# Optimization experiments

Measured on AMD Instinct MI355X. Metric: run time of the kernel, lower is better.

Reference implementation:

```python
import jax, jax.numpy as jnp
import numpy as np

DIM = 64
NUM_EXPERTS = 4
EPS = 1e-6
RESIDUAL_WEIGHT = 0.1
ATTN_SCALE = DIM ** (-0.5)


def setup_inputs() -> dict:
    key = jax.random.key(0)
    ks = jax.random.split(key, 24)
    N, d = 8192, DIM
    w = lambda k, shape: jax.random.normal(k, shape, dtype=jnp.float32) * 0.05
    return {
        "z_real": jax.random.normal(ks[0], (N, d), dtype=jnp.float32),
        "z_imag": jax.random.normal(ks[1], (N, d), dtype=jnp.float32),
        # ComplexMoE
        "gate_W": w(ks[2], (NUM_EXPERTS, 2 * d)),
        "gate_b": jnp.zeros((NUM_EXPERTS,), jnp.float32),
        "exp_Wr": w(ks[3], (NUM_EXPERTS, d, d)),
        "exp_Wi": w(ks[4], (NUM_EXPERTS, d, d)),
        # ComplexLayerNorm
        "ln_scale": jnp.ones((d,), jnp.float32),
        "ln_shift": jnp.zeros((d,), jnp.float32),
        # ModReLU
        "mod_bias": jnp.zeros((d,), jnp.float32),
        # ContextAwareAttention
        "q_Wr": w(ks[5], (d, d)), "q_Wi": w(ks[6], (d, d)),
        "k_Wr": w(ks[7], (d, d)), "k_Wi": w(ks[8], (d, d)),
        "v_Wr": w(ks[9], (d, d)), "v_Wi": w(ks[10], (d, d)),
        "ctx_W": w(ks[11], (2 * d, 2 * d)),
        "ctx_b": jnp.zeros((2 * d,), jnp.float32),
        # residual / halt / stack heads
        "res_W": w(ks[12], (2 * d, 2 * d)),
        "res_b": jnp.zeros((2 * d,), jnp.float32),
        "halt_W": w(ks[13], (1, 2 * d)),
        "halt_b": jnp.full((1,), 2.0, jnp.float32),
        "stack_W": w(ks[14], (3, 2 * d)),
        "stack_b": jnp.zeros((3,), jnp.float32),
    }


def _clinear(xr, xi, Wr, Wi):
    # complex linear: (xr + i xi) @ (Wr + i Wi)^T
    rr = xr @ Wr.T - xi @ Wi.T
    ri = xi @ Wr.T + xr @ Wi.T
    return rr, ri


def reference(z_real, z_imag, gate_W, gate_b, exp_Wr, exp_Wi,
              ln_scale, ln_shift, mod_bias,
              q_Wr, q_Wi, k_Wr, k_Wi, v_Wr, v_Wi, ctx_W, ctx_b,
              res_W, res_b, halt_W, halt_b, stack_W, stack_b):
    d = DIM
    zf = jnp.concatenate([z_real, z_imag], axis=-1)  # [N, 2d]

    # --- ComplexMoE ---
    gw = jax.nn.softmax(zf @ gate_W.T + gate_b, axis=-1)  # [N, E]
    er = jnp.einsum('nd,ekd->nek', z_real, exp_Wr) - jnp.einsum('nd,ekd->nek', z_imag, exp_Wi)
    ei = jnp.einsum('nd,ekd->nek', z_imag, exp_Wr) + jnp.einsum('nd,ekd->nek', z_real, exp_Wi)
    mr = jnp.einsum('ne,nek->nk', gw, er)
    mi = jnp.einsum('ne,nek->nk', gw, ei)

    # --- ComplexLayerNorm (mag stats with unbiased var, phase preserved) ---
    mag = jnp.sqrt(mr * mr + mi * mi) + EPS
    mean = jnp.mean(mag, axis=-1, keepdims=True)
    var = jnp.var(mag, axis=-1, keepdims=True, ddof=1)
    nm = (mag - mean) / jnp.sqrt(var + EPS) * ln_scale + ln_shift
    phase = jnp.arctan2(mi, mr)
    lr = nm * jnp.cos(phase)
    li = nm * jnp.sin(phase)

    # --- ModReLU ---
    nrm = jnp.sqrt(lr * lr + li * li) + EPS
    s = jax.nn.relu(nrm + mod_bias) / nrm
    ar, ai = lr * s, li * s

    # --- ContextAwareAttention (context = original z) ---
    qr, qi = _clinear(ar, ai, q_Wr, q_Wi)
    kr, ki = _clinear(ar, ai, k_Wr, k_Wi)
    vr, vi = _clinear(ar, ai, v_Wr, v_Wi)
    qf = jnp.concatenate([qr, qi], axis=-1)
    cw = jax.nn.sigmoid(zf @ ctx_W.T + ctx_b)
    qf = qf * cw
    kf = jnp.concatenate([kr, ki], axis=-1)
    attn = jax.nn.softmax((qf @ kf.T) * ATTN_SCALE, axis=-1)  # [N, N]
    or_ = attn @ vr
    oi_ = attn @ vi

    # --- residual projection ---
    res = zf @ res_W.T + res_b
    pr = or_ + RESIDUAL_WEIGHT * res[..., :d]
    pi = oi_ + RESIDUAL_WEIGHT * res[..., d:]

    # --- halt / stack heads on L2-normalized flat state ---
    zf2 = jnp.concatenate([pr, pi], axis=-1)
    zn = zf2 / (jnp.linalg.norm(zf2, axis=-1, keepdims=True) + 1e-6)
    halt_logit = zn @ halt_W.T + halt_b
    stack_logits = zn @ stack_W.T + stack_b
    return pr, pi, halt_logit, stack_logits
```

## Files before the change

kernel.cpp:

```cpp
#include <hip/hip_runtime.h>
#include <math.h>

#define EPS_F 1e-6f
#define NCH   8
#define CHUNK 1024
#define TILES 32
#define QSC   (0.125f * 1.44269504088896340736f)

#define GATE_O 0
#define EWR_O  512
#define EWI_O  16896
#define QWR_O  33280
#define QWI_O  37376
#define KWR_O  41472
#define KWI_O  45568
#define VWR_O  49664
#define VWI_O  53760
#define CTX_O  57856
#define RES_O  74240
#define WTOT   90624

typedef __attribute__((ext_vector_type(8))) short short8;
typedef __attribute__((ext_vector_type(4))) float f32x4;
typedef unsigned short ushort_t;
typedef unsigned int uint_t;

__device__ __forceinline__ ushort_t f2bf(float x){
  uint_t u = __float_as_uint(x);
  u += 0x7fffu + ((u >> 16) & 1u);
  return (ushort_t)(u >> 16);
}
__device__ __forceinline__ float bf2f(ushort_t u){
  return __uint_as_float(((uint_t)u) << 16);
}
__device__ __forceinline__ uint_t pack2bf(float lo, float hi){
  return (uint_t)f2bf(lo) | ((uint_t)f2bf(hi) << 16);
}

__device__ __forceinline__ float wave_sum64(float v){
  #pragma unroll
  for (int m = 32; m > 0; m >>= 1) v += __shfl_xor(v, m, 64);
  return v;
}
__device__ __forceinline__ float qsum16(float v){
  #pragma unroll
  for (int m = 1; m < 16; m <<= 1) v += __shfl_xor(v, m, 64);
  return v;
}

__device__ __forceinline__ short8 neg8(short8 v){
  uint4 u = *reinterpret_cast<uint4*>(&v);
  u.x ^= 0x80008000u; u.y ^= 0x80008000u; u.z ^= 0x80008000u; u.w ^= 0x80008000u;
  return *reinterpret_cast<short8*>(&u);
}
__device__ __forceinline__ short8 ld8(const ushort_t* __restrict__ p){
  return *reinterpret_cast<const short8*>(p);
}

#define MFMA(a,b,c) __builtin_amdgcn_mfma_f32_16x16x32_bf16((a),(b),(c),0,0,0)

__global__ __launch_bounds__(256) void wconv_kernel(
    const float* __restrict__ gate_W, const float* __restrict__ exp_Wr,
    const float* __restrict__ exp_Wi,
    const float* __restrict__ q_Wr, const float* __restrict__ q_Wi,
    const float* __restrict__ k_Wr, const float* __restrict__ k_Wi,
    const float* __restrict__ v_Wr, const float* __restrict__ v_Wi,
    const float* __restrict__ ctx_W, const float* __restrict__ res_W,
    ushort_t* __restrict__ whi, ushort_t* __restrict__ wlo)
{
  int i = blockIdx.x * 256 + threadIdx.x;
  if (i >= WTOT) return;
  float v;
  if      (i < EWR_O) v = gate_W[i - GATE_O];
  else if (i < EWI_O) v = exp_Wr[i - EWR_O];
  else if (i < QWR_O) v = exp_Wi[i - EWI_O];
  else if (i < QWI_O) v = q_Wr[i - QWR_O];
  else if (i < KWR_O) v = q_Wi[i - QWI_O];
  else if (i < KWI_O) v = k_Wr[i - KWR_O];
  else if (i < VWR_O) v = k_Wi[i - KWI_O];
  else if (i < VWI_O) v = v_Wr[i - VWR_O];
  else if (i < CTX_O) v = v_Wi[i - VWI_O];
  else if (i < RES_O) v = ctx_W[i - CTX_O];
  else                v = res_W[i - RES_O];
  ushort_t h = f2bf(v);
  whi[i] = h;
  wlo[i] = f2bf(v - bf2f(h));
}

__global__ __launch_bounds__(256, 4) void prep_kernel(
    const float* __restrict__ z_real, const float* __restrict__ z_imag,
    const ushort_t* __restrict__ whi, const ushort_t* __restrict__ wlo,
    const float* __restrict__ gate_b,
    const float* __restrict__ ln_scale, const float* __restrict__ ln_shift,
    const float* __restrict__ mod_bias,
    const float* __restrict__ ctx_b, const float* __restrict__ res_b,
    ushort_t* __restrict__ qf, ushort_t* __restrict__ kf, ushort_t* __restrict__ vt,
    float* __restrict__ resb)
{
  const int tid  = threadIdx.x;
  const int lane = tid & 63;
  const int w    = tid >> 6;
  const int g    = lane >> 4;
  const int c    = lane & 15;
  const int row0 = blockIdx.x * 16;
  const int col  = w * 16 + c;
  const f32x4 z4 = {0.f, 0.f, 0.f, 0.f};

  __shared__ ushort_t s_xh[16][136];
  __shared__ ushort_t s_xl[16][136];
  __shared__ ushort_t s_a [16][136];
  __shared__ ushort_t s_tv[128][20];
  __shared__ float    s_red[4][16][2];

  {
    int rowl = tid >> 4;
    int col0 = (tid & 15) * 8;
    const float* src = (col0 < 64) ? (z_real + (size_t)(row0 + rowl) * 64 + col0)
                                   : (z_imag + (size_t)(row0 + rowl) * 64 + (col0 - 64));
    float4 a = *reinterpret_cast<const float4*>(src);
    float4 b = *reinterpret_cast<const float4*>(src + 4);
    float f[8] = {a.x, a.y, a.z, a.w, b.x, b.y, b.z, b.w};
    uint_t hp[4], lp[4];
    #pragma unroll
    for (int e = 0; e < 4; ++e){
      ushort_t h0 = f2bf(f[2*e]), h1 = f2bf(f[2*e+1]);
      hp[e] = (uint_t)h0 | ((uint_t)h1 << 16);
      lp[e] = (uint_t)f2bf(f[2*e]   - bf2f(h0)) |
              ((uint_t)f2bf(f[2*e+1] - bf2f(h1)) << 16);
    }
    uint4 uh; uh.x = hp[0]; uh.y = hp[1]; uh.z = hp[2]; uh.w = hp[3];
    uint4 ul; ul.x = lp[0]; ul.y = lp[1]; ul.z = lp[2]; ul.w = lp[3];
    *reinterpret_cast<uint4*>(&s_xh[rowl][col0]) = uh;
    *reinterpret_cast<uint4*>(&s_xl[rowl][col0]) = ul;
  }
  __syncthreads();

  short8 xh[4], xl[4];
  #pragma unroll
  for (int ks = 0; ks < 4; ++ks){
    xh[ks] = ld8(&s_xh[c][ks * 32 + g * 8]);
    xl[ks] = ld8(&s_xl[c][ks * 32 + g * 8]);
  }

  float gwv[4];
  {
    f32x4 ga = z4;
    #pragma unroll
    for (int ks = 0; ks < 4; ++ks){
      int off = GATE_O + (c & 3) * 128 + ks * 32 + g * 8;
      short8 wh = ld8(whi + off), wl = ld8(wlo + off);
      ga = MFMA(xh[ks], wh, ga);
      ga = MFMA(xl[ks], wh, ga);
      ga = MFMA(xh[ks], wl, ga);
    }
    float gb = gate_b[c & 3];
    #pragma unroll
    for (int r = 0; r < 4; ++r){
      float le = ga[r] + gb;
      float mx = fmaxf(le, __shfl_xor(le, 1, 64));
      mx = fmaxf(mx, __shfl_xor(mx, 2, 64));
      float ev = __expf(le - mx);
      float sm = ev + __shfl_xor(ev, 1, 64);
      sm += __shfl_xor(sm, 2, 64);
      gwv[r] = ev / sm;
    }
  }

  f32x4 mrr = z4, mri = z4;
  #pragma unroll
  for (int e = 0; e < 4; ++e){
    float gwr[4];
    #pragma unroll
    for (int r = 0; r < 4; ++r) gwr[r] = __shfl(gwv[r], g * 16 + e, 64);
    f32x4 er = z4, ei = z4;
    #pragma unroll
    for (int ks = 0; ks < 2; ++ks){
      int boff = e * 4096 + col * 64 + ks * 32 + g * 8;
      short8 wrh = ld8(whi + EWR_O + boff);
      short8 wrl = ld8(wlo + EWR_O + boff);
      short8 wih = ld8(whi + EWI_O + boff);
      short8 wil = ld8(wlo + EWI_O + boff);
      short8 wihn = neg8(wih), wiln = neg8(wil);
      er = MFMA(xh[ks],   wrh, er);   ei = MFMA(xh[ks+2], wrh, ei);
      er = MFMA(xl[ks],   wrh, er);   ei = MFMA(xl[ks+2], wrh, ei);
      er = MFMA(xh[ks],   wrl, er);   ei = MFMA(xh[ks+2], wrl, ei);
      er = MFMA(xh[ks+2], wihn, er);  ei = MFMA(xh[ks],   wih, ei);
      er = MFMA(xl[ks+2], wihn, er);  ei = MFMA(xl[ks],   wih, ei);
      er = MFMA(xh[ks+2], wiln, er);  ei = MFMA(xh[ks],   wil, ei);
    }
    #pragma unroll
    for (int r = 0; r < 4; ++r){
      mrr[r] = fmaf(gwr[r], er[r], mrr[r]);
      mri[r] = fmaf(gwr[r], ei[r], mri[r]);
    }
  }

  {
    float hh[4], mg[4];
    #pragma unroll
    for (int r = 0; r < 4; ++r){
      hh[r] = sqrtf(mrr[r] * mrr[r] + mri[r] * mri[r]);
      mg[r] = hh[r] + EPS_F;
    }
    #pragma unroll
    for (int r = 0; r < 4; ++r){
      float sx  = qsum16(mg[r]);
      float sxx = qsum16(mg[r] * mg[r]);
      if (c == 0){ s_red[w][g * 4 + r][0] = sx; s_red[w][g * 4 + r][1] = sxx; }
    }
    __syncthreads();
    float lsc = ln_scale[col], lsh = ln_shift[col], mb = mod_bias[col];
    #pragma unroll
    for (int r = 0; r < 4; ++r){
      int rr = g * 4 + r;
      float SX  = s_red[0][rr][0] + s_red[1][rr][0] + s_red[2][rr][0] + s_red[3][rr][0];
      float SXX = s_red[0][rr][1] + s_red[1][rr][1] + s_red[2][rr][1] + s_red[3][rr][1];
      float mean = SX * (1.0f / 64.0f);
      float var  = (SXX - SX * mean) * (1.0f / 63.0f);
      float istd = rsqrtf(var + EPS_F);
      float nm = (mg[r] - mean) * istd * lsc + lsh;
      float lr, li;
      if (hh[r] > 0.f){ float ih = 1.0f / hh[r]; lr = nm * mrr[r] * ih; li = nm * mri[r] * ih; }
      else            { lr = nm; li = 0.f; }
      float nrm = sqrtf(lr * lr + li * li) + EPS_F;
      float sf  = fmaxf(nrm + mb, 0.f) / nrm;
      s_a[rr][col]      = f2bf(lr * sf);
      s_a[rr][64 + col] = f2bf(li * sf);
    }
  }
  __syncthreads();

  f32x4 cwa[2];
  #pragma unroll
  for (int ii = 0; ii < 2; ++ii){
    int ct8 = w + ii * 4;
    f32x4 a = z4;
    #pragma unroll
    for (int ks = 0; ks < 4; ++ks)
      a = MFMA(xh[ks], ld8(whi + CTX_O + (ct8 * 16 + c) * 128 + ks * 32 + g * 8), a);
    float cb = ctx_b[ct8 * 16 + c];
    #pragma unroll
    for (int r = 0; r < 4; ++r) cwa[ii][r] = 1.0f / (1.0f + __expf(-(a[r] + cb)));
  }

  #pragma unroll
  for (int ii = 0; ii < 2; ++ii){
    int ct8 = w + ii * 4;
    f32x4 a = z4;
    #pragma unroll
    for (int ks = 0; ks < 4; ++ks)
      a = MFMA(xh[ks], ld8(whi + RES_O + (ct8 * 16 + c) * 128 + ks * 32 + g * 8), a);
    float rb = res_b[ct8 * 16 + c];
    #pragma unroll
    for (int r = 0; r < 4; ++r)
      resb[(size_t)(row0 + 4 * g + r) * 128 + ct8 * 16 + c] = 0.1f * (a[r] + rb);
  }

  short8 ar_[2], ai_[2], ain_[2];
  #pragma unroll
  for (int ks = 0; ks < 2; ++ks){
    ar_[ks]  = ld8(&s_a[c][ks * 32 + g * 8]);
    ai_[ks]  = ld8(&s_a[c][64 + ks * 32 + g * 8]);
    ain_[ks] = neg8(ai_[ks]);
  }

  #pragma unroll
  for (int mat = 0; mat < 3; ++mat){
    int roff = (mat == 0) ? QWR_O : (mat == 1) ? KWR_O : VWR_O;
    int ioff = (mat == 0) ? QWI_O : (mat == 1) ? KWI_O : VWI_O;
    f32x4 orr = z4, oii = z4;
    #pragma unroll
    for (int ks = 0; ks < 2; ++ks){
      int boff = col * 64 + ks * 32 + g * 8;
      short8 wrh = ld8(whi + roff + boff);
      short8 wrl = ld8(wlo + roff + boff);
      short8 wih = ld8(whi + ioff + boff);
      short8 wil = ld8(wlo + ioff + boff);
      orr = MFMA(ar_[ks],  wrh, orr);  oii = MFMA(ai_[ks], wrh, oii);
      orr = MFMA(ar_[ks],  wrl, orr);  oii = MFMA(ai_[ks], wrl, oii);
      orr = MFMA(ain_[ks], wih, orr);  oii = MFMA(ar_[ks], wih, oii);
      orr = MFMA(ain_[ks], wil, orr);  oii = MFMA(ar_[ks], wil, oii);
    }
    if (mat == 0){
      #pragma unroll
      for (int r = 0; r < 4; ++r){
        size_t row = row0 + 4 * g + r;
        qf[row * 128 + col]      = f2bf(orr[r] * cwa[0][r] * QSC);
        qf[row * 128 + 64 + col] = f2bf(oii[r] * cwa[1][r] * QSC);
      }
    } else if (mat == 1){
      #pragma unroll
      for (int r = 0; r < 4; ++r){
        size_t row = row0 + 4 * g + r;
        kf[row * 128 + col]      = f2bf(orr[r]);
        kf[row * 128 + 64 + col] = f2bf(oii[r]);
      }
    } else {
      #pragma unroll
      for (int r = 0; r < 4; ++r){
        s_tv[col][4 * g + r]      = f2bf(orr[r]);
        s_tv[64 + col][4 * g + r] = f2bf(oii[r]);
      }
    }
  }
  __syncthreads();

  {
    int d = tid >> 1, half = tid & 1;
    uint2 t0 = *reinterpret_cast<const uint2*>(&s_tv[d][half * 8]);
    uint2 t1 = *reinterpret_cast<const uint2*>(&s_tv[d][half * 8 + 4]);
    uint4 o; o.x = t0.x; o.y = t0.y; o.z = t1.x; o.w = t1.y;
    *reinterpret_cast<uint4*>(vt + (size_t)d * 8192 + row0 + half * 8) = o;
  }
}

__global__ __launch_bounds__(256, 4) void attn_mfma(
    const ushort_t* __restrict__ qf, const ushort_t* __restrict__ kf, const ushort_t* __restrict__ vt,
    ushort_t* __restrict__ pacc, float* __restrict__ pm, float* __restrict__ pl)
{
  const int tid  = threadIdx.x;
  const int lane = tid & 63;
  const int w    = tid >> 6;
  const int g    = lane >> 4;
  const int hl   = lane & 15;
  const int qb   = blockIdx.x & 127;
  const int jc   = blockIdx.x >> 7;
  const int q0   = qb * 64;
  const int qr   = q0 + w * 16 + hl;

  __shared__ ushort_t s_k[32][136];
  __shared__ ushort_t s_vt[128][40];
  __shared__ uint_t   s_p32[4][16][20];

  const int kjj0 = tid >> 4;
  const int kkk  = (tid & 15) * 8;
  const int vd0  = tid >> 2;
  const int vjo  = (tid & 3) * 8;

  short8 qfrag[4];
  #pragma unroll
  for (int kt = 0; kt < 4; ++kt)
    qfrag[kt] = *reinterpret_cast<const short8*>(qf + (size_t)qr * 128 + kt * 32 + g * 8);

  f32x4 oacc[8];
  #pragma unroll
  for (int dt = 0; dt < 8; ++dt) oacc[dt] = (f32x4){0.f, 0.f, 0.f, 0.f};
  float mrun = -3.0e38f, lrun = 0.f;

  const int jstart = jc * CHUNK;

  for (int t = 0; t < TILES; ++t){
    const int jb = jstart + t * 32;
    __syncthreads();
    #pragma unroll
    for (int i = 0; i < 2; ++i){
      *reinterpret_cast<uint4*>(&s_k[kjj0 + i * 16][kkk]) =
          *reinterpret_cast<const uint4*>(kf + (size_t)(jb + kjj0 + i * 16) * 128 + kkk);
      *reinterpret_cast<uint4*>(&s_vt[vd0 + i * 64][vjo]) =
          *reinterpret_cast<const uint4*>(vt + (size_t)(vd0 + i * 64) * 8192 + jb + vjo);
    }
    __syncthreads();

    f32x4 sacc[2];
    #pragma unroll
    for (int jt = 0; jt < 2; ++jt){
      sacc[jt] = (f32x4){0.f, 0.f, 0.f, 0.f};
      #pragma unroll
      for (int kt = 0; kt < 4; ++kt){
        short8 kfr = *reinterpret_cast<const short8*>(&s_k[jt * 16 + hl][kt * 32 + g * 8]);
        sacc[jt] = __builtin_amdgcn_mfma_f32_16x16x32_bf16(kfr, qfrag[kt], sacc[jt], 0, 0, 0);
      }
    }

    float t0 = fmaxf(fmaxf(fmaxf(sacc[0][0], sacc[0][1]), fmaxf(sacc[0][2], sacc[0][3])),
                     fmaxf(fmaxf(sacc[1][0], sacc[1][1]), fmaxf(sacc[1][2], sacc[1][3])));
    t0 = fmaxf(t0, __shfl_xor(t0, 16, 64));
    t0 = fmaxf(t0, __shfl_xor(t0, 32, 64));
    if (__any(t0 > mrun)){
      float mnew = fmaxf(mrun, t0);
      float fac  = exp2f(mrun - mnew);
      lrun *= fac;
      #pragma unroll
      for (int dt = 0; dt < 8; ++dt){
        oacc[dt][0] *= fac; oacc[dt][1] *= fac; oacc[dt][2] *= fac; oacc[dt][3] *= fac;
      }
      mrun = mnew;
    }
    float pe[2][4];
    float ps = 0.f;
    #pragma unroll
    for (int jt = 0; jt < 2; ++jt)
      #pragma unroll
      for (int r = 0; r < 4; ++r){
        float p = exp2f(sacc[jt][r] - mrun);
        pe[jt][r] = p;
        ps += p;
      }
    ps += __shfl_xor(ps, 16, 64);
    ps += __shfl_xor(ps, 32, 64);
    lrun += ps;

    {
      uint2 w0; w0.x = pack2bf(pe[0][0], pe[0][1]); w0.y = pack2bf(pe[0][2], pe[0][3]);
      uint2 w1; w1.x = pack2bf(pe[1][0], pe[1][1]); w1.y = pack2bf(pe[1][2], pe[1][3]);
      *reinterpret_cast<uint2*>(&s_p32[w][hl][2 * g])     = w0;
      *reinterpret_cast<uint2*>(&s_p32[w][hl][8 + 2 * g]) = w1;
    }
    short8 pfrag = *reinterpret_cast<const short8*>(&s_p32[w][hl][4 * g]);

    #pragma unroll
    for (int dt = 0; dt < 8; ++dt){
      short8 vfr = *reinterpret_cast<const short8*>(&s_vt[dt * 16 + hl][g * 8]);
      oacc[dt] = __builtin_amdgcn_mfma_f32_16x16x32_bf16(vfr, pfrag, oacc[dt], 0, 0, 0);
    }
  }

  #pragma unroll
  for (int dt = 0; dt < 8; ++dt){
    uint2 o;
    o.x = pack2bf(oacc[dt][0], oacc[dt][1]);
    o.y = pack2bf(oacc[dt][2], oacc[dt][3]);
    *reinterpret_cast<uint2*>(pacc + ((size_t)jc * 8192 + qr) * 128 + dt * 16 + 4 * g) = o;
  }
  if (g == 0){
    pm[jc * 8192 + qr] = mrun;
    pl[jc * 8192 + qr] = lrun;
  }
}

__global__ __launch_bounds__(256, 1) void combine_kernel(
    const ushort_t* __restrict__ pacc, const float* __restrict__ pm, const float* __restrict__ pl,
    const float* __restrict__ resb,
    const float* __restrict__ halt_W, const float* __restrict__ halt_b,
    const float* __restrict__ stack_W, const float* __restrict__ stack_b,
    float* __restrict__ out)
{
  const int tid  = threadIdx.x;
  const int lane = tid & 63;
  const int w    = tid >> 6;
  const int q    = blockIdx.x * 4 + w;

  float mv[NCH], M = -3.0e38f;
  #pragma unroll
  for (int c = 0; c < NCH; ++c){ mv[c] = pm[c * 8192 + q]; M = fmaxf(M, mv[c]); }
  float f[NCH]; float L = 0.f;
  #pragma unroll
  for (int c = 0; c < NCH; ++c){ f[c] = exp2f(mv[c] - M); L += pl[c * 8192 + q] * f[c]; }
  float invL = 1.0f / L;

  float o0 = 0.f, o1 = 0.f;
  #pragma unroll
  for (int c = 0; c < NCH; ++c){
    const ushort_t* pa = pacc + ((size_t)c * 8192 + q) * 128;
    o0 += bf2f(pa[lane])      * f[c];
    o1 += bf2f(pa[64 + lane]) * f[c];
  }
  o0 = o0 * invL + resb[(size_t)q * 128 + lane];
  o1 = o1 * invL + resb[(size_t)q * 128 + 64 + lane];
  out[(size_t)q * 64 + lane] = o0;
  out[(size_t)8192 * 64 + (size_t)q * 64 + lane] = o1;

  float ssq  = wave_sum64(o0 * o0 + o1 * o1);
  float invn = 1.0f / (sqrtf(ssq) + 1e-6f);
  float zn0 = o0 * invn, zn1 = o1 * invn;
  float hp = wave_sum64(zn0 * halt_W[lane]        + zn1 * halt_W[64 + lane]);
  float s0 = wave_sum64(zn0 * stack_W[lane]       + zn1 * stack_W[64 + lane]);
  float s1 = wave_sum64(zn0 * stack_W[128 + lane] + zn1 * stack_W[192 + lane]);
  float s2 = wave_sum64(zn0 * stack_W[256 + lane] + zn1 * stack_W[320 + lane]);
  if (lane == 0){
    out[1048576 + q] = hp + halt_b[0];
    out[1056768 + (size_t)q * 3 + 0] = s0 + stack_b[0];
    out[1056768 + (size_t)q * 3 + 1] = s1 + stack_b[1];
    out[1056768 + (size_t)q * 3 + 2] = s2 + stack_b[2];
  }
}

extern "C" void kernel_launch(void* const* d_in, const int* in_sizes, int n_in,
                              void* d_out, int out_size, void* d_ws, size_t ws_size,
                              hipStream_t stream){
  const float* z_real  = (const float*)d_in[0];
  const float* z_imag  = (const float*)d_in[1];
  const float* gate_W  = (const float*)d_in[2];
  const float* gate_b  = (const float*)d_in[3];
  const float* exp_Wr  = (const float*)d_in[4];
  const float* exp_Wi  = (const float*)d_in[5];
  const float* ln_scale= (const float*)d_in[6];
  const float* ln_shift= (const float*)d_in[7];
  const float* mod_bias= (const float*)d_in[8];
  const float* q_Wr    = (const float*)d_in[9];
  const float* q_Wi    = (const float*)d_in[10];
  const float* k_Wr    = (const float*)d_in[11];
  const float* k_Wi    = (const float*)d_in[12];
  const float* v_Wr    = (const float*)d_in[13];
  const float* v_Wi    = (const float*)d_in[14];
  const float* ctx_W   = (const float*)d_in[15];
  const float* ctx_b   = (const float*)d_in[16];
  const float* res_W   = (const float*)d_in[17];
  const float* res_b   = (const float*)d_in[18];
  const float* halt_W  = (const float*)d_in[19];
  const float* halt_b  = (const float*)d_in[20];
  const float* stack_W = (const float*)d_in[21];
  const float* stack_b = (const float*)d_in[22];

  ushort_t* qbf = (ushort_t*)d_ws;
  ushort_t* kbf = qbf + (size_t)8192*128;
  ushort_t* vtb = kbf + (size_t)8192*128;
  float* resb = (float*)(vtb + (size_t)8192*128);
  ushort_t* pacc = (ushort_t*)(resb + (size_t)8192*128);
  float* pm   = (float*)(pacc + (size_t)NCH*8192*128);
  float* pl   = pm   + NCH*8192;
  ushort_t* whi = (ushort_t*)(pl + NCH*8192);
  ushort_t* wlo = whi + WTOT;

  wconv_kernel<<<(WTOT + 255) / 256, 256, 0, stream>>>(gate_W, exp_Wr, exp_Wi,
      q_Wr, q_Wi, k_Wr, k_Wi, v_Wr, v_Wi, ctx_W, res_W, whi, wlo);
  prep_kernel<<<512, 256, 0, stream>>>(z_real, z_imag, whi, wlo, gate_b,
      ln_scale, ln_shift, mod_bias, ctx_b, res_b, qbf, kbf, vtb, resb);
  attn_mfma<<<128*NCH, 256, 0, stream>>>(qbf, kbf, vtb, pacc, pm, pl);
  combine_kernel<<<2048, 256, 0, stream>>>(pacc, pm, pl, resb,
      halt_W, halt_b, stack_W, stack_b, (float*)d_out);
}
```

Baseline: 122.3 us.

## Register-prefetch K/V tiles, raise split-K chunks to 16, add MFMA priority hints

The attention kernel now loads the next K/V tile into registers while the current tile is computed, so global latency overlaps with the MFMA work. The key dimension is split into 16 chunks instead of 8 when the workspace is large enough, which doubles the grid to fill more CUs. Occupancy hint is raised from 4 to 6, and s_setprio wraps the MFMA sections. The trade-off is more partial-result traffic and combine work, plus extra register pressure from the prefetch registers.

```diff
diff --git a/kernel.cpp b/kernel.cpp
--- a/kernel.cpp
+++ b/kernel.cpp
@@ -2,9 +2,6 @@
 #include <math.h>
 
 #define EPS_F 1e-6f
-#define NCH   8
-#define CHUNK 1024
-#define TILES 32
 #define QSC   (0.125f * 1.44269504088896340736f)
 
 #define GATE_O 0
@@ -314,10 +311,14 @@
   }
 }
 
-__global__ __launch_bounds__(256, 4) void attn_mfma(
+template<int NCH_T>
+__global__ __launch_bounds__(256, 6) void attn_mfma(
     const ushort_t* __restrict__ qf, const ushort_t* __restrict__ kf, const ushort_t* __restrict__ vt,
     ushort_t* __restrict__ pacc, float* __restrict__ pm, float* __restrict__ pl)
 {
+  constexpr int CHUNK_T = 8192 / NCH_T;
+  constexpr int TILES_T = CHUNK_T / 32;
+
   const int tid  = threadIdx.x;
   const int lane = tid & 63;
   const int w    = tid >> 6;
@@ -336,6 +337,10 @@
   const int kkk  = (tid & 15) * 8;
   const int vd0  = tid >> 2;
   const int vjo  = (tid & 3) * 8;
+  const int jstart = jc * CHUNK_T;
+
+  const ushort_t* kp = kf + (size_t)(jstart + kjj0) * 128 + kkk;
+  const ushort_t* vp = vt + (size_t)vd0 * 8192 + jstart + vjo;
 
   short8 qfrag[4];
   #pragma unroll
@@ -347,21 +352,29 @@
   for (int dt = 0; dt < 8; ++dt) oacc[dt] = (f32x4){0.f, 0.f, 0.f, 0.f};
   float mrun = -3.0e38f, lrun = 0.f;
 
-  const int jstart = jc * CHUNK;
-
-  for (int t = 0; t < TILES; ++t){
-    const int jb = jstart + t * 32;
+  uint4 kreg0 = *reinterpret_cast<const uint4*>(kp);
+  uint4 kreg1 = *reinterpret_cast<const uint4*>(kp + 16 * 128);
+  uint4 vreg0 = *reinterpret_cast<const uint4*>(vp);
+  uint4 vreg1 = *reinterpret_cast<const uint4*>(vp + (size_t)64 * 8192);
+  kp += 32 * 128; vp += 32;
+
+  for (int t = 0; t < TILES_T; ++t){
     __syncthreads();
-    #pragma unroll
-    for (int i = 0; i < 2; ++i){
-      *reinterpret_cast<uint4*>(&s_k[kjj0 + i * 16][kkk]) =
-          *reinterpret_cast<const uint4*>(kf + (size_t)(jb + kjj0 + i * 16) * 128 + kkk);
-      *reinterpret_cast<uint4*>(&s_vt[vd0 + i * 64][vjo]) =
-          *reinterpret_cast<const uint4*>(vt + (size_t)(vd0 + i * 64) * 8192 + jb + vjo);
+    *reinterpret_cast<uint4*>(&s_k[kjj0][kkk])       = kreg0;
+    *reinterpret_cast<uint4*>(&s_k[kjj0 + 16][kkk])  = kreg1;
+    *reinterpret_cast<uint4*>(&s_vt[vd0][vjo])       = vreg0;
+    *reinterpret_cast<uint4*>(&s_vt[vd0 + 64][vjo])  = vreg1;
+    if (t + 1 < TILES_T){
+      kreg0 = *reinterpret_cast<const uint4*>(kp);
+      kreg1 = *reinterpret_cast<const uint4*>(kp + 16 * 128);
+      vreg0 = *reinterpret_cast<const uint4*>(vp);
+      vreg1 = *reinterpret_cast<const uint4*>(vp + (size_t)64 * 8192);
+      kp += 32 * 128; vp += 32;
     }
     __syncthreads();
 
     f32x4 sacc[2];
+    __builtin_amdgcn_s_setprio(1);
     #pragma unroll
     for (int jt = 0; jt < 2; ++jt){
       sacc[jt] = (f32x4){0.f, 0.f, 0.f, 0.f};
@@ -371,6 +384,7 @@
         sacc[jt] = __builtin_amdgcn_mfma_f32_16x16x32_bf16(kfr, qfrag[kt], sacc[jt], 0, 0, 0);
       }
     }
+    __builtin_amdgcn_s_setprio(0);
 
     float t0 = fmaxf(fmaxf(fmaxf(sacc[0][0], sacc[0][1]), fmaxf(sacc[0][2], sacc[0][3])),
                      fmaxf(fmaxf(sacc[1][0], sacc[1][1]), fmaxf(sacc[1][2], sacc[1][3])));
@@ -408,11 +422,13 @@
     }
     short8 pfrag = *reinterpret_cast<const short8*>(&s_p32[w][hl][4 * g]);
 
+    __builtin_amdgcn_s_setprio(1);
     #pragma unroll
     for (int dt = 0; dt < 8; ++dt){
       short8 vfr = *reinterpret_cast<const short8*>(&s_vt[dt * 16 + hl][g * 8]);
       oacc[dt] = __builtin_amdgcn_mfma_f32_16x16x32_bf16(vfr, pfrag, oacc[dt], 0, 0, 0);
     }
+    __builtin_amdgcn_s_setprio(0);
   }
 
   #pragma unroll
@@ -428,6 +444,7 @@
   }
 }
 
+template<int NCH_T>
 __global__ __launch_bounds__(256, 1) void combine_kernel(
     const ushort_t* __restrict__ pacc, const float* __restrict__ pm, const float* __restrict__ pl,
     const float* __restrict__ resb,
@@ -440,17 +457,17 @@
   const int w    = tid >> 6;
   const int q    = blockIdx.x * 4 + w;
 
-  float mv[NCH], M = -3.0e38f;
-  #pragma unroll
-  for (int c = 0; c < NCH; ++c){ mv[c] = pm[c * 8192 + q]; M = fmaxf(M, mv[c]); }
-  float f[NCH]; float L = 0.f;
-  #pragma unroll
-  for (int c = 0; c < NCH; ++c){ f[c] = exp2f(mv[c] - M); L += pl[c * 8192 + q] * f[c]; }
+  float mv[NCH_T], M = -3.0e38f;
+  #pragma unroll
+  for (int c = 0; c < NCH_T; ++c){ mv[c] = pm[c * 8192 + q]; M = fmaxf(M, mv[c]); }
+  float f[NCH_T]; float L = 0.f;
+  #pragma unroll
+  for (int c = 0; c < NCH_T; ++c){ f[c] = exp2f(mv[c] - M); L += pl[c * 8192 + q] * f[c]; }
   float invL = 1.0f / L;
 
   float o0 = 0.f, o1 = 0.f;
   #pragma unroll
-  for (int c = 0; c < NCH; ++c){
+  for (int c = 0; c < NCH_T; ++c){
     const ushort_t* pa = pacc + ((size_t)c * 8192 + q) * 128;
     o0 += bf2f(pa[lane])      * f[c];
     o1 += bf2f(pa[64 + lane]) * f[c];
@@ -502,21 +519,38 @@
   const float* stack_W = (const float*)d_in[21];
   const float* stack_b = (const float*)d_in[22];
 
+  const size_t base_elems = (size_t)3 * 8192 * 128;
+  auto need = [&](int nch)->size_t{
+    size_t b = base_elems * 2;
+    b += (size_t)8192 * 128 * 4;
+    b += (size_t)nch * 8192 * 128 * 2;
+    b += (size_t)2 * nch * 8192 * 4;
+    b += (size_t)2 * WTOT * 2;
+    return b;
+  };
+  const int nch = (ws_size >= need(16)) ? 16 : 8;
+
   ushort_t* qbf = (ushort_t*)d_ws;
   ushort_t* kbf = qbf + (size_t)8192*128;
   ushort_t* vtb = kbf + (size_t)8192*128;
   float* resb = (float*)(vtb + (size_t)8192*128);
   ushort_t* pacc = (ushort_t*)(resb + (size_t)8192*128);
-  float* pm   = (float*)(pacc + (size_t)NCH*8192*128);
-  float* pl   = pm   + NCH*8192;
-  ushort_t* whi = (ushort_t*)(pl + NCH*8192);
+  float* pm   = (float*)(pacc + (size_t)nch*8192*128);
+  float* pl   = pm   + (size_t)nch*8192;
+  ushort_t* whi = (ushort_t*)(pl + (size_t)nch*8192);
   ushort_t* wlo = whi + WTOT;
 
   wconv_kernel<<<(WTOT + 255) / 256, 256, 0, stream>>>(gate_W, exp_Wr, exp_Wi,
       q_Wr, q_Wi, k_Wr, k_Wi, v_Wr, v_Wi, ctx_W, res_W, whi, wlo);
   prep_kernel<<<512, 256, 0, stream>>>(z_real, z_imag, whi, wlo, gate_b,
       ln_scale, ln_shift, mod_bias, ctx_b, res_b, qbf, kbf, vtb, resb);
-  attn_mfma<<<128*NCH, 256, 0, stream>>>(qbf, kbf, vtb, pacc, pm, pl);
-  combine_kernel<<<2048, 256, 0, stream>>>(pacc, pm, pl, resb,
-      halt_W, halt_b, stack_W, stack_b, (float*)d_out);
-}
+  if (nch == 16){
+    attn_mfma<16><<<128*16, 256, 0, stream>>>(qbf, kbf, vtb, pacc, pm, pl);
+    combine_kernel<16><<<2048, 256, 0, stream>>>(pacc, pm, pl, resb,
+        halt_W, halt_b, stack_W, stack_b, (float*)d_out);
+  } else {
+    attn_mfma<8><<<128*8, 256, 0, stream>>>(qbf, kbf, vtb, pacc, pm, pl);
+    combine_kernel<8><<<2048, 256, 0, stream>>>(pacc, pm, pl, resb,
+        halt_W, halt_b, stack_W, stack_b, (float*)d_out);
+  }
+}
```

After: 204.6 us. +67.3%, slower.

## Load K/V MFMA fragments directly from global memory instead of LDS staging

Applied to the files above, without the earlier changes.

The attention kernel no longer stages each K and V^T tile through shared memory. Each wave now reads its MFMA fragments straight from global memory through a helper, which removes the two block-wide barriers per tile and the LDS write/read traffic. It also raises wave priority around the MFMA sections with s_setprio. The trade-off is that all four waves fetch the same K/V data separately, so they rely on cache hits, and load latency is no longer hidden by cooperative staging.

```diff
diff --git a/kernel.cpp b/kernel.cpp
--- a/kernel.cpp
+++ b/kernel.cpp
@@ -328,49 +328,36 @@
   const int q0   = qb * 64;
   const int qr   = q0 + w * 16 + hl;
 
-  __shared__ ushort_t s_k[32][136];
-  __shared__ ushort_t s_vt[128][40];
-  __shared__ uint_t   s_p32[4][16][20];
-
-  const int kjj0 = tid >> 4;
-  const int kkk  = (tid & 15) * 8;
-  const int vd0  = tid >> 2;
-  const int vjo  = (tid & 3) * 8;
+  __shared__ uint_t s_p32[4][16][20];
+
+  const ushort_t* kbase = kf + (size_t)(jc * CHUNK + hl) * 128 + g * 8;
+  const ushort_t* vbase = vt + (size_t)hl * 8192 + jc * CHUNK + g * 8;
 
   short8 qfrag[4];
   #pragma unroll
   for (int kt = 0; kt < 4; ++kt)
-    qfrag[kt] = *reinterpret_cast<const short8*>(qf + (size_t)qr * 128 + kt * 32 + g * 8);
+    qfrag[kt] = ld8(qf + (size_t)qr * 128 + kt * 32 + g * 8);
 
   f32x4 oacc[8];
   #pragma unroll
   for (int dt = 0; dt < 8; ++dt) oacc[dt] = (f32x4){0.f, 0.f, 0.f, 0.f};
   float mrun = -3.0e38f, lrun = 0.f;
 
-  const int jstart = jc * CHUNK;
-
   for (int t = 0; t < TILES; ++t){
-    const int jb = jstart + t * 32;
-    __syncthreads();
-    #pragma unroll
-    for (int i = 0; i < 2; ++i){
-      *reinterpret_cast<uint4*>(&s_k[kjj0 + i * 16][kkk]) =
-          *reinterpret_cast<const uint4*>(kf + (size_t)(jb + kjj0 + i * 16) * 128 + kkk);
-      *reinterpret_cast<uint4*>(&s_vt[vd0 + i * 64][vjo]) =
-          *reinterpret_cast<const uint4*>(vt + (size_t)(vd0 + i * 64) * 8192 + jb + vjo);
-    }
-    __syncthreads();
+    const int jb = t * 32;
 
     f32x4 sacc[2];
+    __builtin_amdgcn_s_setprio(1);
     #pragma unroll
     for (int jt = 0; jt < 2; ++jt){
       sacc[jt] = (f32x4){0.f, 0.f, 0.f, 0.f};
       #pragma unroll
       for (int kt = 0; kt < 4; ++kt){
-        short8 kfr = *reinterpret_cast<const short8*>(&s_k[jt * 16 + hl][kt * 32 + g * 8]);
+        short8 kfr = ld8(kbase + (size_t)(jb + jt * 16) * 128 + kt * 32);
         sacc[jt] = __builtin_amdgcn_mfma_f32_16x16x32_bf16(kfr, qfrag[kt], sacc[jt], 0, 0, 0);
       }
     }
+    __builtin_amdgcn_s_setprio(0);
 
     float t0 = fmaxf(fmaxf(fmaxf(sacc[0][0], sacc[0][1]), fmaxf(sacc[0][2], sacc[0][3])),
                      fmaxf(fmaxf(sacc[1][0], sacc[1][1]), fmaxf(sacc[1][2], sacc[1][3])));
@@ -408,11 +395,13 @@
     }
     short8 pfrag = *reinterpret_cast<const short8*>(&s_p32[w][hl][4 * g]);
 
+    __builtin_amdgcn_s_setprio(1);
     #pragma unroll
     for (int dt = 0; dt < 8; ++dt){
-      short8 vfr = *reinterpret_cast<const short8*>(&s_vt[dt * 16 + hl][g * 8]);
+      short8 vfr = ld8(vbase + (size_t)(dt * 16) * 8192 + jb);
       oacc[dt] = __builtin_amdgcn_mfma_f32_16x16x32_bf16(vfr, pfrag, oacc[dt], 0, 0, 0);
     }
+    __builtin_amdgcn_s_setprio(0);
   }
 
   #pragma unroll
@@ -508,8 +497,8 @@
   float* resb = (float*)(vtb + (size_t)8192*128);
   ushort_t* pacc = (ushort_t*)(resb + (size_t)8192*128);
   float* pm   = (float*)(pacc + (size_t)NCH*8192*128);
-  float* pl   = pm   + NCH*8192;
-  ushort_t* whi = (ushort_t*)(pl + NCH*8192);
+  float* pl   = pm   + (size_t)NCH*8192;
+  ushort_t* whi = (ushort_t*)(pl + (size_t)NCH*8192);
   ushort_t* wlo = whi + WTOT;
 
   wconv_kernel<<<(WTOT + 255) / 256, 256, 0, stream>>>(gate_W, exp_Wr, exp_Wi,
```

After: 272.7 us. 123% more time.
